# Performance work log

Hardware: AMD Instinct MI355X
Metric: run time of the kernel (lower is better)

The kernel has to match this reference:

```python
import jax, jax.numpy as jnp
import numpy as np

N = 40000        # total nodes (2000 graphs x 20 nodes)
E = 60000        # edges per relation (before self-loops)
R = 6            # number of relations
IN = 32
HID = 128
OUT = 128
H = 2            # heads
C = 128          # per-head out channels (concat=False)
B = 2000         # number of graphs
NEG_SLOPE = 0.2


def setup_inputs() -> dict:
    key = jax.random.key(0)
    ks = jax.random.split(key, 16)
    rn = lambda k, s, sc=0.05: (jax.random.normal(k, s, jnp.float32) * sc)
    x = jax.random.normal(ks[0], (N, IN), jnp.float32)
    edge_index = jax.random.randint(ks[1], (R, 2, E), 0, N, dtype=jnp.int32)
    batch = (jnp.arange(N, dtype=jnp.int32) // (N // B)).astype(jnp.int32)
    return {
        "x": x, "edge_index": edge_index, "batch": batch,
        "Wl1": rn(ks[2], (R, IN, H * C)), "bl1": jnp.zeros((R, H * C), jnp.float32),
        "Wr1": rn(ks[3], (R, IN, H * C)), "br1": jnp.zeros((R, H * C), jnp.float32),
        "att1": rn(ks[4], (R, H, C)), "bias1": jnp.zeros((R, C), jnp.float32),
        "Wl2": rn(ks[5], (R, HID, H * C)), "bl2": jnp.zeros((R, H * C), jnp.float32),
        "Wr2": rn(ks[6], (R, HID, H * C)), "br2": jnp.zeros((R, H * C), jnp.float32),
        "att2": rn(ks[7], (R, H, C)), "bias2": jnp.zeros((R, C), jnp.float32),
        "ln1_g": jnp.ones((HID,), jnp.float32), "ln1_b": jnp.zeros((HID,), jnp.float32),
        "ln2_g": jnp.ones((HID,), jnp.float32), "ln2_b": jnp.zeros((HID,), jnp.float32),
        "query": rn(ks[8], (HID,), 0.02),
        "projW": rn(ks[9], (HID, OUT)), "projb": jnp.zeros((OUT,), jnp.float32),
    }


def _gatv2(x, src, dst, Wl, bl, Wr, br, att, bias):
    # x: [N, F]; src/dst: [Etot] (self-loops already appended)
    n = x.shape[0]
    xl = (x @ Wl + bl).reshape(n, H, C)   # source transform
    xr = (x @ Wr + br).reshape(n, H, C)   # target transform
    e = jax.nn.leaky_relu(xl[src] + xr[dst], NEG_SLOPE)   # [Etot, H, C]
    logits = jnp.einsum('ehc,hc->eh', e, att)             # [Etot, H]
    m = jax.ops.segment_max(logits, dst, num_segments=n)
    a = jnp.exp(logits - m[dst])
    s = jax.ops.segment_sum(a, dst, num_segments=n)
    w = a / s[dst]                                        # segment softmax
    out = jax.ops.segment_sum(w[:, :, None] * xl[src], dst, num_segments=n)
    return out.mean(axis=1) + bias                        # head-average (concat=False)


def _hetero_layer(x, edge_index, Wl, bl, Wr, br, att, bias):
    loops = jnp.broadcast_to(jnp.arange(N, dtype=edge_index.dtype), (R, N))
    src = jnp.concatenate([edge_index[:, 0, :], loops], axis=1)  # [R, E+N]
    dst = jnp.concatenate([edge_index[:, 1, :], loops], axis=1)
    outs = jax.vmap(_gatv2, in_axes=(None, 0, 0, 0, 0, 0, 0, 0, 0))(
        x, src, dst, Wl, bl, Wr, br, att, bias)
    return outs.sum(axis=0)  # HeteroConv aggr='sum'


def _layernorm(x, g, b, eps=1e-5):
    mu = x.mean(-1, keepdims=True)
    var = ((x - mu) ** 2).mean(-1, keepdims=True)
    return (x - mu) * jax.lax.rsqrt(var + eps) * g + b


def reference(x, edge_index, batch, Wl1, bl1, Wr1, br1, att1, bias1,
              Wl2, bl2, Wr2, br2, att2, bias2,
              ln1_g, ln1_b, ln2_g, ln2_b, query, projW, projb):
    h = _hetero_layer(x, edge_index, Wl1, bl1, Wr1, br1, att1, bias1)
    h = _layernorm(jnp.tanh(h), ln1_g, ln1_b)
    h = _hetero_layer(h, edge_index, Wl2, bl2, Wr2, br2, att2, bias2)
    h = _layernorm(jnp.tanh(h), ln2_g, ln2_b)
    # attention pooling over graphs (segment softmax on batch ids)
    scores = h @ query                              # [N]
    m = jax.ops.segment_max(scores, batch, num_segments=B)
    a = jnp.exp(scores - m[batch])
    s = jax.ops.segment_sum(a, batch, num_segments=B)
    w = a / s[batch]
    g = jax.ops.segment_sum(w[:, None] * h, batch, num_segments=B)  # [B, HID]
    return g @ projW + projb
```

## Files before the change

kernel.cpp:

```cpp
#include <hip/hip_runtime.h>
#include <hip/hip_bf16.h>
#include <math.h>

#define N_NODES 40000
#define E_EDGES 60000
#define R_REL 6
#define IN_F 32
#define HID_F 128
#define B_GRAPHS 2000
#define NODES_PER_G 20
#define NEG_SLOPE 0.2f
#define NB (R_REL * N_NODES)
#define NTOT (R_REL * (E_EDGES + N_NODES))
#define NBLK ((NB + 255) / 256)

typedef __bf16 bf16x8 __attribute__((ext_vector_type(8)));
typedef float f32x4 __attribute__((ext_vector_type(4)));

__device__ __forceinline__ unsigned f2bfbits(float f) {
    unsigned u = __builtin_bit_cast(unsigned, f);
    return (u + 0x7FFFu + ((u >> 16) & 1u)) >> 16;
}
__device__ __forceinline__ float bflo(unsigned u) { return __builtin_bit_cast(float, u << 16); }
__device__ __forceinline__ float bfhi(unsigned u) { return __builtin_bit_cast(float, u & 0xFFFF0000u); }

__global__ __launch_bounds__(256) void count_kernel(
    const int* __restrict__ ei, int* __restrict__ cnt)
{
    int idx = blockIdx.x * 256 + threadIdx.x;
    if (idx >= NTOT) return;
    int bin;
    if (idx < R_REL * E_EDGES) {
        int r = idx / E_EDGES, e = idx - r * E_EDGES;
        bin = r * N_NODES + ei[(size_t)r * 2 * E_EDGES + E_EDGES + e];
    } else {
        bin = idx - R_REL * E_EDGES;
    }
    atomicAdd(&cnt[bin], 1);
}

__global__ __launch_bounds__(256) void scan1_kernel(
    const int* __restrict__ cnt, int* __restrict__ part, int* __restrict__ bsum)
{
    int i = blockIdx.x * 256 + threadIdx.x;
    int v = (i < NB) ? cnt[i] : 0;
    int lane = threadIdx.x & 63, w = threadIdx.x >> 6;
    int x = v;
#pragma unroll
    for (int off = 1; off < 64; off <<= 1) {
        int y = __shfl_up(x, off, 64);
        if (lane >= off) x += y;
    }
    __shared__ int ws[4];
    if (lane == 63) ws[w] = x;
    __syncthreads();
    int add = 0;
    for (int j = 0; j < w; j++) add += ws[j];
    int incl = x + add;
    if (i < NB) part[i] = incl - v;
    if (threadIdx.x == 255) bsum[blockIdx.x] = incl;
}

__global__ __launch_bounds__(1024) void scan2_kernel(
    const int* __restrict__ bsum, int* __restrict__ boff)
{
    __shared__ int buf[1024];
    int t = threadIdx.x;
    int v0 = (t < NBLK) ? bsum[t] : 0;
    buf[t] = v0;
    __syncthreads();
    for (int off = 1; off < 1024; off <<= 1) {
        int v = (t >= off) ? buf[t - off] : 0;
        __syncthreads();
        buf[t] += v;
        __syncthreads();
    }
    if (t < NBLK) boff[t] = buf[t] - v0;
}

__global__ __launch_bounds__(256) void scan3_kernel(
    const int* __restrict__ part, const int* __restrict__ boff,
    int* __restrict__ rowptr, int* __restrict__ cursor)
{
    int i = blockIdx.x * 256 + threadIdx.x;
    if (i < NB) {
        int v = part[i] + boff[i >> 8];
        rowptr[i] = v;
        cursor[i] = v;
    }
    if (i == 0) rowptr[NB] = NTOT;
}

__global__ __launch_bounds__(256) void scatter_kernel(
    const int* __restrict__ ei, int* __restrict__ cursor, int* __restrict__ csr)
{
    int idx = blockIdx.x * 256 + threadIdx.x;
    if (idx >= NTOT) return;
    int bin, src;
    if (idx < R_REL * E_EDGES) {
        int r = idx / E_EDGES, e = idx - r * E_EDGES;
        src = ei[(size_t)r * 2 * E_EDGES + e];
        bin = r * N_NODES + ei[(size_t)r * 2 * E_EDGES + E_EDGES + e];
    } else {
        bin = idx - R_REL * E_EDGES;
        src = bin % N_NODES;
    }
    int pos = atomicAdd(&cursor[bin], 1);
    csr[pos] = src;
}

__global__ __launch_bounds__(256) void cvt_bf16_kernel(
    const float* __restrict__ src, unsigned* __restrict__ dst, int npairs)
{
    int i = blockIdx.x * 256 + threadIdx.x;
    if (i >= npairs) return;
    float2 v = *(const float2*)(src + 2 * i);
    dst[i] = f2bfbits(v.x) | (f2bfbits(v.y) << 16);
}

__global__ __launch_bounds__(256) void prep_w_kernel(
    const float* __restrict__ Wl, const float* __restrict__ Wr,
    const float* __restrict__ bl, const float* __restrict__ br,
    unsigned short* __restrict__ Bt, float* __restrict__ bcat, int K)
{
    int idx = blockIdx.x * 256 + threadIdx.x;
    if (idx >= R_REL * 512 * K) return;
    int k = idx % K;
    int rn = idx / K;
    int n = rn % 512;
    int r = rn / 512;
    int nn = n & 255;
    const float* W = (n < 256) ? Wl : Wr;
    float w = W[((size_t)r * K + k) * 256 + nn];
    Bt[idx] = (unsigned short)f2bfbits(w);
    if (k == 0)
        bcat[rn] = (n < 256) ? bl[r * 256 + nn] : br[r * 256 + nn];
}

template <int K>
__global__ __launch_bounds__(256, 4) void gemm_mfma_kernel(
    const unsigned short* __restrict__ A,
    const unsigned short* __restrict__ BtAll,
    const float* __restrict__ biasAll,
    unsigned short* __restrict__ CAll)
{
    constexpr int KC = (K > 64) ? 64 : K;
    constexpr int NCH = K / KC;
    constexpr int CH = KC / 8;
    constexpr int TB = 128 * KC * 2;
    __shared__ char lds[2 * TB];
    char* ldsA = lds;
    char* ldsB = lds + TB;

    int tid = threadIdx.x;
    int lane = tid & 63, wave = tid >> 6;
    int l16 = lane & 15, quad = lane >> 4;
    int wm = (wave >> 1) * 64, wn = (wave & 1) * 64;
    int ny = blockIdx.x & 3, z = blockIdx.x >> 2;
    int m0 = blockIdx.y * 128, n0 = ny * 128;

    auto SW = [](int row) { return (KC == 64) ? (row & 7) : ((row >> 1) & 3); };

    const char* Bt = (const char*)(BtAll + (size_t)z * 512 * K);

    f32x4 acc[4][4];
#pragma unroll
    for (int i = 0; i < 4; i++)
#pragma unroll
        for (int j = 0; j < 4; j++) {
            acc[i][j][0] = 0.f; acc[i][j][1] = 0.f;
            acc[i][j][2] = 0.f; acc[i][j][3] = 0.f;
        }

    for (int nc = 0; nc < NCH; ++nc) {
        if (nc) __syncthreads();
#pragma unroll
        for (int it = 0; it < (128 * CH) / 256; ++it) {
            int s = it * 256 + tid;
            int row = s / CH, sc = s % CH;
            int c = sc ^ SW(row);
            int gr = m0 + row; gr = gr < N_NODES ? gr : N_NODES - 1;
            const char* gpA = (const char*)A + (size_t)gr * (K * 2) + nc * KC * 2 + c * 16;
            __builtin_amdgcn_global_load_lds(
                (const __attribute__((address_space(1))) void*)gpA,
                (__attribute__((address_space(3))) void*)(ldsA + it * 4096 + wave * 1024), 16, 0, 0);
            const char* gpB = Bt + (size_t)(n0 + row) * (K * 2) + nc * KC * 2 + c * 16;
            __builtin_amdgcn_global_load_lds(
                (const __attribute__((address_space(1))) void*)gpB,
                (__attribute__((address_space(3))) void*)(ldsB + it * 4096 + wave * 1024), 16, 0, 0);
        }
        __syncthreads();

#pragma unroll
        for (int kk = 0; kk < KC / 32; ++kk) {
            bf16x8 af[4], bfr[4];
#pragma unroll
            for (int i = 0; i < 4; ++i) {
                int row = wm + i * 16 + l16;
                int slot = (kk * 4 + quad) ^ SW(row);
                af[i] = *(const bf16x8*)(ldsA + row * (KC * 2) + slot * 16);
            }
#pragma unroll
            for (int j = 0; j < 4; ++j) {
                int row = wn + j * 16 + l16;
                int slot = (kk * 4 + quad) ^ SW(row);
                bfr[j] = *(const bf16x8*)(ldsB + row * (KC * 2) + slot * 16);
            }
#pragma unroll
            for (int i = 0; i < 4; i++)
#pragma unroll
                for (int j = 0; j < 4; j++)
                    acc[i][j] = __builtin_amdgcn_mfma_f32_16x16x32_bf16(af[i], bfr[j], acc[i][j], 0, 0, 0);
        }
    }

    const float* bias = biasAll + z * 512;
    unsigned short* C = CAll + (size_t)z * N_NODES * 512;
    float biasj[4];
#pragma unroll
    for (int j = 0; j < 4; ++j) biasj[j] = bias[n0 + wn + j * 16 + l16];
#pragma unroll
    for (int i = 0; i < 4; i++) {
        int gr0 = m0 + wm + i * 16 + quad * 4;
#pragma unroll
        for (int j = 0; j < 4; j++) {
            int col = n0 + wn + j * 16 + l16;
#pragma unroll
            for (int rg = 0; rg < 4; rg++) {
                float a = acc[i][j][rg] + biasj[j];
                float b = __shfl_xor(a, 1);
                int grow = gr0 + rg;
                if (!(lane & 1) && grow < N_NODES) {
                    __hip_bfloat162 h2 = __float22bfloat162_rn(make_float2(a, b));
                    unsigned u;
                    __builtin_memcpy(&u, &h2, 4);
                    *(unsigned*)((char*)C + ((size_t)grow * 512 + col) * 2) = u;
                }
            }
        }
    }
}

__global__ __launch_bounds__(256) void gat6_ln_kernel(
    const unsigned short* __restrict__ XLR,
    const int* __restrict__ rowptr,
    const int* __restrict__ csr,
    const float* __restrict__ att,
    const float* __restrict__ bias,
    const float* __restrict__ lng, const float* __restrict__ lnb,
    unsigned* __restrict__ hout)
{
    int gtid = blockIdx.x * 256 + threadIdx.x;
    int d = gtid >> 6;
    int lane = threadIdx.x & 63;
    if (d >= N_NODES) return;
    int hl = lane & 31;

    float tot0 = 0.f, tot1 = 0.f, tot2 = 0.f, tot3 = 0.f;
#pragma unroll 1
    for (int r = 0; r < R_REL; r++) {
        const char* base = (const char*)XLR + (size_t)r * N_NODES * 1024;
        const unsigned* xrp = (const unsigned*)(base + (size_t)d * 1024 + 512 + lane * 8);
        unsigned xu0 = xrp[0], xu1 = xrp[1];
        float xr0 = bflo(xu0), xr1 = bfhi(xu0), xr2 = bflo(xu1), xr3 = bfhi(xu1);
        float4 av = *(const float4*)(att + r * 256 + lane * 4);

        int bin = r * N_NODES + d;
        int beg = __builtin_amdgcn_readfirstlane(rowptr[bin]);
        int end = __builtin_amdgcn_readfirstlane(rowptr[bin + 1]);

        float sA = 0.f, a0 = 0.f, a1 = 0.f, a2 = 0.f, a3 = 0.f;
        float sB = 0.f, b0 = 0.f, b1 = 0.f, b2 = 0.f, b3 = 0.f;
        int i = beg;
        for (; i + 2 <= end; i += 2) {
            int s0 = csr[i], s1 = csr[i + 1];
            const unsigned* pA = (const unsigned*)(base + (size_t)s0 * 1024 + lane * 8);
            const unsigned* pB = (const unsigned*)(base + (size_t)s1 * 1024 + lane * 8);
            unsigned uA0 = pA[0], uA1 = pA[1];
            unsigned uB0 = pB[0], uB1 = pB[1];
            float xA0 = bflo(uA0), xA1 = bfhi(uA0), xA2 = bflo(uA1), xA3 = bfhi(uA1);
            float xB0 = bflo(uB0), xB1 = bfhi(uB0), xB2 = bflo(uB1), xB3 = bfhi(uB1);
            float tA0 = xA0 + xr0, tA1 = xA1 + xr1, tA2 = xA2 + xr2, tA3 = xA3 + xr3;
            float tB0 = xB0 + xr0, tB1 = xB1 + xr1, tB2 = xB2 + xr2, tB3 = xB3 + xr3;
            tA0 = fmaxf(tA0, NEG_SLOPE * tA0); tB0 = fmaxf(tB0, NEG_SLOPE * tB0);
            tA1 = fmaxf(tA1, NEG_SLOPE * tA1); tB1 = fmaxf(tB1, NEG_SLOPE * tB1);
            tA2 = fmaxf(tA2, NEG_SLOPE * tA2); tB2 = fmaxf(tB2, NEG_SLOPE * tB2);
            tA3 = fmaxf(tA3, NEG_SLOPE * tA3); tB3 = fmaxf(tB3, NEG_SLOPE * tB3);
            float pa = tA0 * av.x + tA1 * av.y + tA2 * av.z + tA3 * av.w;
            float pb = tB0 * av.x + tB1 * av.y + tB2 * av.z + tB3 * av.w;
            pa += __shfl_xor(pa, 16); pb += __shfl_xor(pb, 16);
            pa += __shfl_xor(pa, 8);  pb += __shfl_xor(pb, 8);
            pa += __shfl_xor(pa, 4);  pb += __shfl_xor(pb, 4);
            pa += __shfl_xor(pa, 2);  pb += __shfl_xor(pb, 2);
            pa += __shfl_xor(pa, 1);  pb += __shfl_xor(pb, 1);
            float wa = __expf(fminf(pa, 60.f));
            float wb = __expf(fminf(pb, 60.f));
            sA += wa; sB += wb;
            a0 = fmaf(wa, xA0, a0); b0 = fmaf(wb, xB0, b0);
            a1 = fmaf(wa, xA1, a1); b1 = fmaf(wb, xB1, b1);
            a2 = fmaf(wa, xA2, a2); b2 = fmaf(wb, xB2, b2);
            a3 = fmaf(wa, xA3, a3); b3 = fmaf(wb, xB3, b3);
        }
        if (i < end) {
            int s0 = csr[i];
            const unsigned* pA = (const unsigned*)(base + (size_t)s0 * 1024 + lane * 8);
            unsigned uA0 = pA[0], uA1 = pA[1];
            float xA0 = bflo(uA0), xA1 = bfhi(uA0), xA2 = bflo(uA1), xA3 = bfhi(uA1);
            float tA0 = xA0 + xr0, tA1 = xA1 + xr1, tA2 = xA2 + xr2, tA3 = xA3 + xr3;
            tA0 = fmaxf(tA0, NEG_SLOPE * tA0);
            tA1 = fmaxf(tA1, NEG_SLOPE * tA1);
            tA2 = fmaxf(tA2, NEG_SLOPE * tA2);
            tA3 = fmaxf(tA3, NEG_SLOPE * tA3);
            float pa = tA0 * av.x + tA1 * av.y + tA2 * av.z + tA3 * av.w;
            pa += __shfl_xor(pa, 16);
            pa += __shfl_xor(pa, 8);
            pa += __shfl_xor(pa, 4);
            pa += __shfl_xor(pa, 2);
            pa += __shfl_xor(pa, 1);
            float wa = __expf(fminf(pa, 60.f));
            sA += wa;
            a0 = fmaf(wa, xA0, a0);
            a1 = fmaf(wa, xA1, a1);
            a2 = fmaf(wa, xA2, a2);
            a3 = fmaf(wa, xA3, a3);
        }
        sA += sB; a0 += b0; a1 += b1; a2 += b2; a3 += b3;
        float rs = 0.5f * __builtin_amdgcn_rcpf(sA);
        float o0 = a0 * rs, o1 = a1 * rs, o2 = a2 * rs, o3 = a3 * rs;
        o0 += __shfl_xor(o0, 32);
        o1 += __shfl_xor(o1, 32);
        o2 += __shfl_xor(o2, 32);
        o3 += __shfl_xor(o3, 32);
        float4 bv = *(const float4*)(bias + r * 128 + hl * 4);
        tot0 += o0 + bv.x;
        tot1 += o1 + bv.y;
        tot2 += o2 + bv.z;
        tot3 += o3 + bv.w;
    }
    float v0 = tanhf(tot0), v1 = tanhf(tot1), v2 = tanhf(tot2), v3 = tanhf(tot3);
    float sum = v0 + v1 + v2 + v3;
    float sq = v0 * v0 + v1 * v1 + v2 * v2 + v3 * v3;
#pragma unroll
    for (int off = 16; off >= 1; off >>= 1) {
        sum += __shfl_xor(sum, off);
        sq  += __shfl_xor(sq, off);
    }
    float mean = sum * (1.f / 128.f);
    float var = sq * (1.f / 128.f) - mean * mean;
    float rstd = rsqrtf(var + 1e-5f);
    float4 gg = *(const float4*)(lng + hl * 4);
    float4 bb = *(const float4*)(lnb + hl * 4);
    float o0 = (v0 - mean) * rstd * gg.x + bb.x;
    float o1 = (v1 - mean) * rstd * gg.y + bb.y;
    float o2 = (v2 - mean) * rstd * gg.z + bb.z;
    float o3 = (v3 - mean) * rstd * gg.w + bb.w;
    if (lane < 32) {
        uint2 q;
        q.x = f2bfbits(o0) | (f2bfbits(o1) << 16);
        q.y = f2bfbits(o2) | (f2bfbits(o3) << 16);
        *((uint2*)(hout + (size_t)d * 64) + hl) = q;
    }
}

__global__ __launch_bounds__(256) void pool_kernel(
    const unsigned* __restrict__ hb, const float* __restrict__ query,
    float* __restrict__ gout)
{
    int gtid = blockIdx.x * 256 + threadIdx.x;
    int bg = gtid >> 6;
    int lane = threadIdx.x & 63;
    if (bg >= B_GRAPHS) return;
    float2 q = *(const float2*)(query + 2 * lane);
    float mx = -1e30f, ssum = 0.f, g0 = 0.f, g1 = 0.f;
    for (int i = 0; i < NODES_PER_G; i++) {
        unsigned u = hb[(size_t)(bg * NODES_PER_G + i) * 64 + lane];
        float h0 = bflo(u), h1 = bfhi(u);
        float p = h0 * q.x + h1 * q.y;
#pragma unroll
        for (int off = 32; off >= 1; off >>= 1) p += __shfl_xor(p, off, 64);
        float mn = fmaxf(mx, p);
        float sc = __expf(mx - mn), w = __expf(p - mn);
        ssum = ssum * sc + w;
        g0 = g0 * sc + w * h0;
        g1 = g1 * sc + w * h1;
        mx = mn;
    }
    float2 o; o.x = g0 / ssum; o.y = g1 / ssum;
    *(float2*)(gout + (size_t)bg * 128 + 2 * lane) = o;
}

__global__ __launch_bounds__(128) void proj_kernel(
    const float* __restrict__ g, const float* __restrict__ W,
    const float* __restrict__ bias, float* __restrict__ out)
{
    int bg = blockIdx.x;
    int o = threadIdx.x;
    const float* gp = g + (size_t)bg * 128;
    float acc = bias[o];
    for (int k = 0; k < 128; k++) acc = fmaf(gp[k], W[k * 128 + o], acc);
    out[(size_t)bg * 128 + o] = acc;
}

extern "C" void kernel_launch(void* const* d_in, const int* in_sizes, int n_in,
                              void* d_out, int out_size, void* d_ws, size_t ws_size,
                              hipStream_t stream)
{
    const float* x     = (const float*)d_in[0];
    const int*   ei    = (const int*)d_in[1];
    const float* Wl1   = (const float*)d_in[3];
    const float* bl1   = (const float*)d_in[4];
    const float* Wr1   = (const float*)d_in[5];
    const float* br1   = (const float*)d_in[6];
    const float* att1  = (const float*)d_in[7];
    const float* bias1 = (const float*)d_in[8];
    const float* Wl2   = (const float*)d_in[9];
    const float* bl2   = (const float*)d_in[10];
    const float* Wr2   = (const float*)d_in[11];
    const float* br2   = (const float*)d_in[12];
    const float* att2  = (const float*)d_in[13];
    const float* bias2 = (const float*)d_in[14];
    const float* ln1g  = (const float*)d_in[15];
    const float* ln1b  = (const float*)d_in[16];
    const float* ln2g  = (const float*)d_in[17];
    const float* ln2b  = (const float*)d_in[18];
    const float* query = (const float*)d_in[19];
    const float* projW = (const float*)d_in[20];
    const float* projb = (const float*)d_in[21];
    float* out = (float*)d_out;

    unsigned short* xlr6 = (unsigned short*)d_ws;
    unsigned short* h1bf = xlr6 + (size_t)R_REL * N_NODES * 512;
    unsigned short* xbf  = h1bf + (size_t)N_NODES * 128;
    unsigned short* Bt1  = xbf + (size_t)N_NODES * 32;
    unsigned short* Bt2  = Bt1 + R_REL * 512 * 32;
    float* bc1  = (float*)(Bt2 + R_REL * 512 * 128);
    float* bc2  = bc1 + R_REL * 512;
    float* gb   = bc2 + R_REL * 512;
    int* cnt    = (int*)(gb + (size_t)B_GRAPHS * 128);
    int* part   = cnt + NB;
    int* rowptr = part + NB;
    int* cursor = rowptr + NB + 1;
    int* bsum   = cursor + NB;
    int* boff   = bsum + NBLK;
    int* csr    = boff + NBLK;

    hipMemsetAsync(cnt, 0, sizeof(int) * NB, stream);
    count_kernel<<<(NTOT + 255) / 256, 256, 0, stream>>>(ei, cnt);
    scan1_kernel<<<NBLK, 256, 0, stream>>>(cnt, part, bsum);
    scan2_kernel<<<1, 1024, 0, stream>>>(bsum, boff);
    scan3_kernel<<<NBLK, 256, 0, stream>>>(part, boff, rowptr, cursor);
    scatter_kernel<<<(NTOT + 255) / 256, 256, 0, stream>>>(ei, cursor, csr);

    cvt_bf16_kernel<<<(N_NODES * 16 + 255) / 256, 256, 0, stream>>>(x, (unsigned*)xbf, N_NODES * 16);
    prep_w_kernel<<<(R_REL * 512 * 32 + 255) / 256, 256, 0, stream>>>(Wl1, Wr1, bl1, br1, Bt1, bc1, 32);
    prep_w_kernel<<<(R_REL * 512 * 128 + 255) / 256, 256, 0, stream>>>(Wl2, Wr2, bl2, br2, Bt2, bc2, 128);

    dim3 ggrid(24, (N_NODES + 127) / 128, 1);
    gemm_mfma_kernel<32><<<ggrid, 256, 0, stream>>>(xbf, Bt1, bc1, xlr6);
    gat6_ln_kernel<<<N_NODES / 4, 256, 0, stream>>>(
        xlr6, rowptr, csr, att1, bias1, ln1g, ln1b, (unsigned*)h1bf);
    gemm_mfma_kernel<128><<<ggrid, 256, 0, stream>>>(h1bf, Bt2, bc2, xlr6);
    gat6_ln_kernel<<<N_NODES / 4, 256, 0, stream>>>(
        xlr6, rowptr, csr, att2, bias2, ln2g, ln2b, (unsigned*)h1bf);
    pool_kernel<<<B_GRAPHS / 4, 256, 0, stream>>>((unsigned*)h1bf, query, gb);
    proj_kernel<<<B_GRAPHS, 128, 0, stream>>>(gb, projW, projb, out);
}
```

Measured before the change: 466.4 us.

## Split GAT wavefront into two half-waves each processing alternate edges with 16-byte loads

Restructures the per-node GATv2 aggregation so each 64-lane wavefront runs two independent 32-lane halves. Each half handles every other incoming edge, and each lane loads 8 bf16 channels (16 bytes) instead of 4. This cuts the per-edge shuffle reduction from five steps to four, raises load width, and replaces the serial pair-plus-tail loop with a predicated strided loop. The per-relation bias add is also folded into a precomputed summed bias from a small new kernel. The cost is more cross-lane reductions at the end and masked wasted work when a node has an odd edge count.

Measured after the change: 483.3 us. 3.6% more time.

```diff
diff --git a/kernel.cpp b/kernel.cpp
--- a/kernel.cpp
+++ b/kernel.cpp
@@ -135,6 +135,16 @@
     Bt[idx] = (unsigned short)f2bfbits(w);
     if (k == 0)
         bcat[rn] = (n < 256) ? bl[r * 256 + nn] : br[r * 256 + nn];
+}
+
+__global__ __launch_bounds__(128) void bias_sum_kernel(
+    const float* __restrict__ b1, const float* __restrict__ b2,
+    float* __restrict__ o1, float* __restrict__ o2)
+{
+    int c = threadIdx.x;
+    float s1 = 0.f, s2 = 0.f;
+    for (int r = 0; r < R_REL; r++) { s1 += b1[r * 128 + c]; s2 += b2[r * 128 + c]; }
+    o1[c] = s1; o2[c] = s2;
 }
 
 template <int K>
@@ -246,119 +256,116 @@
     const int* __restrict__ rowptr,
     const int* __restrict__ csr,
     const float* __restrict__ att,
-    const float* __restrict__ bias,
+    const float* __restrict__ biasSum,
     const float* __restrict__ lng, const float* __restrict__ lnb,
     unsigned* __restrict__ hout)
 {
-    int gtid = blockIdx.x * 256 + threadIdx.x;
-    int d = gtid >> 6;
     int lane = threadIdx.x & 63;
-    if (d >= N_NODES) return;
+    int wv = __builtin_amdgcn_readfirstlane(threadIdx.x) >> 6;
+    int d = blockIdx.x * 4 + wv;
+    int eh = lane >> 5;
     int hl = lane & 31;
+    int cs = hl & 15;
 
     float tot0 = 0.f, tot1 = 0.f, tot2 = 0.f, tot3 = 0.f;
+    float tot4 = 0.f, tot5 = 0.f, tot6 = 0.f, tot7 = 0.f;
+
 #pragma unroll 1
     for (int r = 0; r < R_REL; r++) {
         const char* base = (const char*)XLR + (size_t)r * N_NODES * 1024;
-        const unsigned* xrp = (const unsigned*)(base + (size_t)d * 1024 + 512 + lane * 8);
-        unsigned xu0 = xrp[0], xu1 = xrp[1];
-        float xr0 = bflo(xu0), xr1 = bfhi(xu0), xr2 = bflo(xu1), xr3 = bfhi(xu1);
-        float4 av = *(const float4*)(att + r * 256 + lane * 4);
+        uint4 xru = *(const uint4*)(base + (size_t)d * 1024 + 512 + hl * 16);
+        float xr0 = bflo(xru.x), xr1 = bfhi(xru.x), xr2 = bflo(xru.y), xr3 = bfhi(xru.y);
+        float xr4 = bflo(xru.z), xr5 = bfhi(xru.z), xr6 = bflo(xru.w), xr7 = bfhi(xru.w);
+        float4 a0 = *(const float4*)(att + r * 256 + hl * 8);
+        float4 a1 = *(const float4*)(att + r * 256 + hl * 8 + 4);
 
         int bin = r * N_NODES + d;
-        int beg = __builtin_amdgcn_readfirstlane(rowptr[bin]);
-        int end = __builtin_amdgcn_readfirstlane(rowptr[bin + 1]);
-
-        float sA = 0.f, a0 = 0.f, a1 = 0.f, a2 = 0.f, a3 = 0.f;
-        float sB = 0.f, b0 = 0.f, b1 = 0.f, b2 = 0.f, b3 = 0.f;
-        int i = beg;
-        for (; i + 2 <= end; i += 2) {
-            int s0 = csr[i], s1 = csr[i + 1];
-            const unsigned* pA = (const unsigned*)(base + (size_t)s0 * 1024 + lane * 8);
-            const unsigned* pB = (const unsigned*)(base + (size_t)s1 * 1024 + lane * 8);
-            unsigned uA0 = pA[0], uA1 = pA[1];
-            unsigned uB0 = pB[0], uB1 = pB[1];
-            float xA0 = bflo(uA0), xA1 = bfhi(uA0), xA2 = bflo(uA1), xA3 = bfhi(uA1);
-            float xB0 = bflo(uB0), xB1 = bfhi(uB0), xB2 = bflo(uB1), xB3 = bfhi(uB1);
-            float tA0 = xA0 + xr0, tA1 = xA1 + xr1, tA2 = xA2 + xr2, tA3 = xA3 + xr3;
-            float tB0 = xB0 + xr0, tB1 = xB1 + xr1, tB2 = xB2 + xr2, tB3 = xB3 + xr3;
-            tA0 = fmaxf(tA0, NEG_SLOPE * tA0); tB0 = fmaxf(tB0, NEG_SLOPE * tB0);
-            tA1 = fmaxf(tA1, NEG_SLOPE * tA1); tB1 = fmaxf(tB1, NEG_SLOPE * tB1);
-            tA2 = fmaxf(tA2, NEG_SLOPE * tA2); tB2 = fmaxf(tB2, NEG_SLOPE * tB2);
-            tA3 = fmaxf(tA3, NEG_SLOPE * tA3); tB3 = fmaxf(tB3, NEG_SLOPE * tB3);
-            float pa = tA0 * av.x + tA1 * av.y + tA2 * av.z + tA3 * av.w;
-            float pb = tB0 * av.x + tB1 * av.y + tB2 * av.z + tB3 * av.w;
-            pa += __shfl_xor(pa, 16); pb += __shfl_xor(pb, 16);
-            pa += __shfl_xor(pa, 8);  pb += __shfl_xor(pb, 8);
-            pa += __shfl_xor(pa, 4);  pb += __shfl_xor(pb, 4);
-            pa += __shfl_xor(pa, 2);  pb += __shfl_xor(pb, 2);
-            pa += __shfl_xor(pa, 1);  pb += __shfl_xor(pb, 1);
-            float wa = __expf(fminf(pa, 60.f));
-            float wb = __expf(fminf(pb, 60.f));
-            sA += wa; sB += wb;
-            a0 = fmaf(wa, xA0, a0); b0 = fmaf(wb, xB0, b0);
-            a1 = fmaf(wa, xA1, a1); b1 = fmaf(wb, xB1, b1);
-            a2 = fmaf(wa, xA2, a2); b2 = fmaf(wb, xB2, b2);
-            a3 = fmaf(wa, xA3, a3); b3 = fmaf(wb, xB3, b3);
+        int beg = rowptr[bin];
+        int end = rowptr[bin + 1];
+
+        float s = 0.f;
+        float c0 = 0.f, c1 = 0.f, c2 = 0.f, c3 = 0.f;
+        float c4 = 0.f, c5 = 0.f, c6 = 0.f, c7 = 0.f;
+        int nit = (end - beg + 1) >> 1;
+        int idx = beg + eh;
+        for (int t = 0; t < nit; ++t, idx += 2) {
+            int valid = idx < end;
+            int src = csr[valid ? idx : beg];
+            uint4 u = *(const uint4*)(base + (size_t)src * 1024 + hl * 16);
+            float x0 = bflo(u.x), x1 = bfhi(u.x), x2 = bflo(u.y), x3 = bfhi(u.y);
+            float x4 = bflo(u.z), x5 = bfhi(u.z), x6 = bflo(u.w), x7 = bfhi(u.w);
+            float t0 = x0 + xr0, t1 = x1 + xr1, t2 = x2 + xr2, t3 = x3 + xr3;
+            float t4 = x4 + xr4, t5 = x5 + xr5, t6 = x6 + xr6, t7 = x7 + xr7;
+            t0 = fmaxf(t0, NEG_SLOPE * t0); t1 = fmaxf(t1, NEG_SLOPE * t1);
+            t2 = fmaxf(t2, NEG_SLOPE * t2); t3 = fmaxf(t3, NEG_SLOPE * t3);
+            t4 = fmaxf(t4, NEG_SLOPE * t4); t5 = fmaxf(t5, NEG_SLOPE * t5);
+            t6 = fmaxf(t6, NEG_SLOPE * t6); t7 = fmaxf(t7, NEG_SLOPE * t7);
+            float p = t0 * a0.x;
+            p = fmaf(t1, a0.y, p); p = fmaf(t2, a0.z, p); p = fmaf(t3, a0.w, p);
+            p = fmaf(t4, a1.x, p); p = fmaf(t5, a1.y, p); p = fmaf(t6, a1.z, p);
+            p = fmaf(t7, a1.w, p);
+            p += __shfl_xor(p, 8);
+            p += __shfl_xor(p, 4);
+            p += __shfl_xor(p, 2);
+            p += __shfl_xor(p, 1);
+            float w = valid ? __expf(fminf(p, 60.f)) : 0.f;
+            s += w;
+            c0 = fmaf(w, x0, c0); c1 = fmaf(w, x1, c1);
+            c2 = fmaf(w, x2, c2); c3 = fmaf(w, x3, c3);
+            c4 = fmaf(w, x4, c4); c5 = fmaf(w, x5, c5);
+            c6 = fmaf(w, x6, c6); c7 = fmaf(w, x7, c7);
         }
-        if (i < end) {
-            int s0 = csr[i];
-            const unsigned* pA = (const unsigned*)(base + (size_t)s0 * 1024 + lane * 8);
-            unsigned uA0 = pA[0], uA1 = pA[1];
-            float xA0 = bflo(uA0), xA1 = bfhi(uA0), xA2 = bflo(uA1), xA3 = bfhi(uA1);
-            float tA0 = xA0 + xr0, tA1 = xA1 + xr1, tA2 = xA2 + xr2, tA3 = xA3 + xr3;
-            tA0 = fmaxf(tA0, NEG_SLOPE * tA0);
-            tA1 = fmaxf(tA1, NEG_SLOPE * tA1);
-            tA2 = fmaxf(tA2, NEG_SLOPE * tA2);
-            tA3 = fmaxf(tA3, NEG_SLOPE * tA3);
-            float pa = tA0 * av.x + tA1 * av.y + tA2 * av.z + tA3 * av.w;
-            pa += __shfl_xor(pa, 16);
-            pa += __shfl_xor(pa, 8);
-            pa += __shfl_xor(pa, 4);
-            pa += __shfl_xor(pa, 2);
-            pa += __shfl_xor(pa, 1);
-            float wa = __expf(fminf(pa, 60.f));
-            sA += wa;
-            a0 = fmaf(wa, xA0, a0);
-            a1 = fmaf(wa, xA1, a1);
-            a2 = fmaf(wa, xA2, a2);
-            a3 = fmaf(wa, xA3, a3);
-        }
-        sA += sB; a0 += b0; a1 += b1; a2 += b2; a3 += b3;
-        float rs = 0.5f * __builtin_amdgcn_rcpf(sA);
-        float o0 = a0 * rs, o1 = a1 * rs, o2 = a2 * rs, o3 = a3 * rs;
-        o0 += __shfl_xor(o0, 32);
-        o1 += __shfl_xor(o1, 32);
-        o2 += __shfl_xor(o2, 32);
-        o3 += __shfl_xor(o3, 32);
-        float4 bv = *(const float4*)(bias + r * 128 + hl * 4);
-        tot0 += o0 + bv.x;
-        tot1 += o1 + bv.y;
-        tot2 += o2 + bv.z;
-        tot3 += o3 + bv.w;
-    }
-    float v0 = tanhf(tot0), v1 = tanhf(tot1), v2 = tanhf(tot2), v3 = tanhf(tot3);
-    float sum = v0 + v1 + v2 + v3;
-    float sq = v0 * v0 + v1 * v1 + v2 * v2 + v3 * v3;
-#pragma unroll
-    for (int off = 16; off >= 1; off >>= 1) {
+        s += __shfl_xor(s, 32);
+        float rs = 0.5f * __builtin_amdgcn_rcpf(s);
+        tot0 = fmaf(c0, rs, tot0); tot1 = fmaf(c1, rs, tot1);
+        tot2 = fmaf(c2, rs, tot2); tot3 = fmaf(c3, rs, tot3);
+        tot4 = fmaf(c4, rs, tot4); tot5 = fmaf(c5, rs, tot5);
+        tot6 = fmaf(c6, rs, tot6); tot7 = fmaf(c7, rs, tot7);
+    }
+    tot0 += __shfl_xor(tot0, 32); tot1 += __shfl_xor(tot1, 32);
+    tot2 += __shfl_xor(tot2, 32); tot3 += __shfl_xor(tot3, 32);
+    tot4 += __shfl_xor(tot4, 32); tot5 += __shfl_xor(tot5, 32);
+    tot6 += __shfl_xor(tot6, 32); tot7 += __shfl_xor(tot7, 32);
+    tot0 += __shfl_xor(tot0, 16); tot1 += __shfl_xor(tot1, 16);
+    tot2 += __shfl_xor(tot2, 16); tot3 += __shfl_xor(tot3, 16);
+    tot4 += __shfl_xor(tot4, 16); tot5 += __shfl_xor(tot5, 16);
+    tot6 += __shfl_xor(tot6, 16); tot7 += __shfl_xor(tot7, 16);
+    float4 bs0 = *(const float4*)(biasSum + cs * 8);
+    float4 bs1 = *(const float4*)(biasSum + cs * 8 + 4);
+    float v0 = tanhf(tot0 + bs0.x), v1 = tanhf(tot1 + bs0.y);
+    float v2 = tanhf(tot2 + bs0.z), v3 = tanhf(tot3 + bs0.w);
+    float v4 = tanhf(tot4 + bs1.x), v5 = tanhf(tot5 + bs1.y);
+    float v6 = tanhf(tot6 + bs1.z), v7 = tanhf(tot7 + bs1.w);
+    float sum = v0 + v1 + v2 + v3 + v4 + v5 + v6 + v7;
+    float sq = v0 * v0 + v1 * v1 + v2 * v2 + v3 * v3
+             + v4 * v4 + v5 * v5 + v6 * v6 + v7 * v7;
+#pragma unroll
+    for (int off = 8; off >= 1; off >>= 1) {
         sum += __shfl_xor(sum, off);
         sq  += __shfl_xor(sq, off);
     }
     float mean = sum * (1.f / 128.f);
     float var = sq * (1.f / 128.f) - mean * mean;
     float rstd = rsqrtf(var + 1e-5f);
-    float4 gg = *(const float4*)(lng + hl * 4);
-    float4 bb = *(const float4*)(lnb + hl * 4);
-    float o0 = (v0 - mean) * rstd * gg.x + bb.x;
-    float o1 = (v1 - mean) * rstd * gg.y + bb.y;
-    float o2 = (v2 - mean) * rstd * gg.z + bb.z;
-    float o3 = (v3 - mean) * rstd * gg.w + bb.w;
-    if (lane < 32) {
-        uint2 q;
+    float4 g0 = *(const float4*)(lng + cs * 8);
+    float4 g1 = *(const float4*)(lng + cs * 8 + 4);
+    float4 b0 = *(const float4*)(lnb + cs * 8);
+    float4 b1 = *(const float4*)(lnb + cs * 8 + 4);
+    float o0 = (v0 - mean) * rstd * g0.x + b0.x;
+    float o1 = (v1 - mean) * rstd * g0.y + b0.y;
+    float o2 = (v2 - mean) * rstd * g0.z + b0.z;
+    float o3 = (v3 - mean) * rstd * g0.w + b0.w;
+    float o4 = (v4 - mean) * rstd * g1.x + b1.x;
+    float o5 = (v5 - mean) * rstd * g1.y + b1.y;
+    float o6 = (v6 - mean) * rstd * g1.z + b1.z;
+    float o7 = (v7 - mean) * rstd * g1.w + b1.w;
+    if (lane < 16) {
+        uint4 q;
         q.x = f2bfbits(o0) | (f2bfbits(o1) << 16);
         q.y = f2bfbits(o2) | (f2bfbits(o3) << 16);
-        *((uint2*)(hout + (size_t)d * 64) + hl) = q;
+        q.z = f2bfbits(o4) | (f2bfbits(o5) << 16);
+        q.w = f2bfbits(o6) | (f2bfbits(o7) << 16);
+        *((uint4*)((char*)hout + (size_t)d * 256) + cs) = q;
     }
 }
 
@@ -436,7 +443,9 @@
     float* bc1  = (float*)(Bt2 + R_REL * 512 * 128);
     float* bc2  = bc1 + R_REL * 512;
     float* gb   = bc2 + R_REL * 512;
-    int* cnt    = (int*)(gb + (size_t)B_GRAPHS * 128);
+    float* bsum1 = gb + (size_t)B_GRAPHS * 128;
+    float* bsum2 = bsum1 + 128;
+    int* cnt    = (int*)(bsum2 + 128);
     int* part   = cnt + NB;
     int* rowptr = part + NB;
     int* cursor = rowptr + NB + 1;
@@ -454,14 +463,15 @@
     cvt_bf16_kernel<<<(N_NODES * 16 + 255) / 256, 256, 0, stream>>>(x, (unsigned*)xbf, N_NODES * 16);
     prep_w_kernel<<<(R_REL * 512 * 32 + 255) / 256, 256, 0, stream>>>(Wl1, Wr1, bl1, br1, Bt1, bc1, 32);
     prep_w_kernel<<<(R_REL * 512 * 128 + 255) / 256, 256, 0, stream>>>(Wl2, Wr2, bl2, br2, Bt2, bc2, 128);
+    bias_sum_kernel<<<1, 128, 0, stream>>>(bias1, bias2, bsum1, bsum2);
 
     dim3 ggrid(24, (N_NODES + 127) / 128, 1);
     gemm_mfma_kernel<32><<<ggrid, 256, 0, stream>>>(xbf, Bt1, bc1, xlr6);
     gat6_ln_kernel<<<N_NODES / 4, 256, 0, stream>>>(
-        xlr6, rowptr, csr, att1, bias1, ln1g, ln1b, (unsigned*)h1bf);
+        xlr6, rowptr, csr, att1, bsum1, ln1g, ln1b, (unsigned*)h1bf);
     gemm_mfma_kernel<128><<<ggrid, 256, 0, stream>>>(h1bf, Bt2, bc2, xlr6);
     gat6_ln_kernel<<<N_NODES / 4, 256, 0, stream>>>(
-        xlr6, rowptr, csr, att2, bias2, ln2g, ln2b, (unsigned*)h1bf);
+        xlr6, rowptr, csr, att2, bsum2, ln2g, ln2b, (unsigned*)h1bf);
     pool_kernel<<<B_GRAPHS / 4, 256, 0, stream>>>((unsigned*)h1bf, query, gb);
     proj_kernel<<<B_GRAPHS, 128, 0, stream>>>(gb, projW, projb, out);
 }
```
